# Performance work log

Measured on AMD Instinct MI355X. Metric: run time of the kernel, lower is better.

The kernel has to match this reference:

```python
import jax, jax.numpy as jnp
import numpy as np

N = 100000       # num nodes
E = 3200000      # num edges (avg degree 32)
F_IN = 128       # num_node_features
HID = 16         # hidden dim hard-coded in Net
C = 10           # num_classes


def setup_inputs() -> dict:
    key = jax.random.key(0)
    k1, k2, k3, k4 = jax.random.split(key, 4)
    x = jax.random.normal(k1, (N, F_IN), dtype=jnp.float32)
    edge_index = jax.random.randint(k2, (2, E), 0, N, dtype=jnp.int32)
    W1 = jax.random.normal(k3, (F_IN, HID), dtype=jnp.float32) * 0.05
    b1 = jnp.zeros((HID,), dtype=jnp.float32)
    W2 = jax.random.normal(k4, (HID, C), dtype=jnp.float32) * 0.05
    b2 = jnp.zeros((C,), dtype=jnp.float32)
    return {"x": x, "edge_index": edge_index, "W1": W1, "b1": b1, "W2": W2, "b2": b2}


def reference(x, edge_index, W1, b1, W2, b2):
    # GCNConv: out = D^{-1/2} (A + I) D^{-1/2} X W + b   (add self-loops)
    loops = jnp.arange(N, dtype=edge_index.dtype)
    row = jnp.concatenate([edge_index[0], loops])  # source nodes
    col = jnp.concatenate([edge_index[1], loops])  # target nodes

    # symmetric normalization (degrees include self-loops, so deg >= 1)
    deg = jax.ops.segment_sum(jnp.ones_like(col, dtype=jnp.float32), col, num_segments=N)
    dis = jax.lax.rsqrt(deg)
    norm = dis[row] * dis[col]  # [E+N]

    def gcn_conv(h, W, b):
        h = h @ W                               # [N, d_out] small GEMM first
        msg = h[row] * norm[:, None]            # gather + scale, [E+N, d_out]
        out = jax.ops.segment_sum(msg, col, num_segments=N)  # scatter-add
        return out + b

    h = jax.nn.relu(gcn_conv(x, W1, b1))
    # F.dropout(training=False) is identity in eval mode
    logits = gcn_conv(h, W2, b2)
    return jax.nn.log_softmax(logits, axis=1)
```

## Files before the change

### kernel.cpp

```cpp
#include <hip/hip_runtime.h>
#include <math.h>

#define N_NODES 100000
#define N_EDGES 3200000
#define F_IN 128
#define HID 16
#define C_OUT 10
#define WIN 256
#define NDIG 391
#define PNB2 500
#define EPB 6400
#define SCN (NDIG * PNB2)
#define SB1 764
#define MAXE 40

typedef unsigned short u16;
typedef unsigned int u32;

__device__ __forceinline__ float bf2f(u16 u) {
    return __uint_as_float(((u32)u) << 16);
}
__device__ __forceinline__ u16 f2bf(float f) {
    u32 x = __float_as_uint(f);
    u32 r = (x + 0x7fffu + ((x >> 16) & 1u)) >> 16;
    return (u16)r;
}
__device__ __forceinline__ void acc8(float* a, uint4 w) {
    a[0] += bf2f((u16)(w.x & 0xffff)); a[1] += bf2f((u16)(w.x >> 16));
    a[2] += bf2f((u16)(w.y & 0xffff)); a[3] += bf2f((u16)(w.y >> 16));
    a[4] += bf2f((u16)(w.z & 0xffff)); a[5] += bf2f((u16)(w.z >> 16));
    a[6] += bf2f((u16)(w.w & 0xffff)); a[7] += bf2f((u16)(w.w >> 16));
}

__global__ void k_pcnt(const int* __restrict__ col, int* __restrict__ blkhistA) {
    __shared__ int h[NDIG];
    for (int i = threadIdx.x; i < NDIG; i += 256) h[i] = 0;
    __syncthreads();
    const uint4* c4 = (const uint4*)(col + blockIdx.x * EPB);
    for (int i = threadIdx.x; i < EPB / 4; i += 256) {
        uint4 c = c4[i];
        atomicAdd(&h[c.x >> 8], 1);
        atomicAdd(&h[c.y >> 8], 1);
        atomicAdd(&h[c.z >> 8], 1);
        atomicAdd(&h[c.w >> 8], 1);
    }
    __syncthreads();
    for (int d = threadIdx.x; d < NDIG; d += 256)
        blkhistA[d * PNB2 + blockIdx.x] = h[d];
}

__global__ void k_s1(const int* __restrict__ blkhistA, int* __restrict__ psum) {
    __shared__ int sm[256];
    int i = blockIdx.x * 256 + threadIdx.x;
    sm[threadIdx.x] = (i < SCN) ? blkhistA[i] : 0;
    __syncthreads();
    for (int off = 128; off > 0; off >>= 1) {
        if (threadIdx.x < off) sm[threadIdx.x] += sm[threadIdx.x + off];
        __syncthreads();
    }
    if (threadIdx.x == 0) psum[blockIdx.x] = sm[0];
}

__global__ void k_s3(const int* __restrict__ blkhistA, const int* __restrict__ psum,
                     int* __restrict__ blkhistB) {
    __shared__ int ps[1024];
    __shared__ int sm[256];
    int t = threadIdx.x;
    for (int i = t; i < 1024; i += 256) ps[i] = (i < SB1) ? psum[i] : 0;
    __syncthreads();
    for (int off = 1; off < 1024; off <<= 1) {
        int v[4];
#pragma unroll
        for (int j = 0; j < 4; j++) {
            int idx = t + j * 256;
            v[j] = ps[idx] + ((idx >= off) ? ps[idx - off] : 0);
        }
        __syncthreads();
#pragma unroll
        for (int j = 0; j < 4; j++) ps[t + j * 256] = v[j];
        __syncthreads();
    }
    int bpre = (blockIdx.x > 0) ? ps[blockIdx.x - 1] : 0;

    int i = blockIdx.x * 256 + t;
    int v = (i < SCN) ? blkhistA[i] : 0;
    sm[t] = v;
    __syncthreads();
    for (int off = 1; off < 256; off <<= 1) {
        int a = sm[t];
        int b = (t >= off) ? sm[t - off] : 0;
        __syncthreads();
        sm[t] = a + b;
        __syncthreads();
    }
    if (i < SCN) blkhistB[i] = bpre + sm[t] - v;
}

__global__ void __launch_bounds__(512) k_pwrite(
        const int* __restrict__ row, const int* __restrict__ col,
        const int* __restrict__ blkhistA, const int* __restrict__ blkhistB,
        u32* __restrict__ staging) {
    __shared__ u32 sorted[EPB];
    __shared__ u16 dwin[EPB];
    __shared__ int gbase[NDIG];
    __shared__ int lbase[NDIG];
    __shared__ int lcur[NDIG];
    __shared__ int scan[512];

    int t = threadIdx.x;
    int b = blockIdx.x;
    int hv = 0;
    if (t < NDIG) {
        hv = blkhistA[t * PNB2 + b];
        gbase[t] = blkhistB[t * PNB2 + b];
        lcur[t] = 0;
    }
    scan[t] = hv;
    __syncthreads();
    for (int off = 1; off < 512; off <<= 1) {
        int v = scan[t];
        int u = (t >= off) ? scan[t - off] : 0;
        __syncthreads();
        scan[t] = v + u;
        __syncthreads();
    }
    if (t < NDIG) lbase[t] = scan[t] - hv;
    __syncthreads();

    const uint4* c4 = (const uint4*)(col + b * EPB);
    const uint4* r4 = (const uint4*)(row + b * EPB);
    for (int i = t; i < EPB / 4; i += 512) {
        uint4 c = c4[i];
        uint4 r = r4[i];
        int d, rank, pos;
        d = (int)(c.x >> 8); rank = atomicAdd(&lcur[d], 1); pos = lbase[d] + rank;
        sorted[pos] = ((c.x & 255u) << 17) | r.x; dwin[pos] = (u16)d;
        d = (int)(c.y >> 8); rank = atomicAdd(&lcur[d], 1); pos = lbase[d] + rank;
        sorted[pos] = ((c.y & 255u) << 17) | r.y; dwin[pos] = (u16)d;
        d = (int)(c.z >> 8); rank = atomicAdd(&lcur[d], 1); pos = lbase[d] + rank;
        sorted[pos] = ((c.z & 255u) << 17) | r.z; dwin[pos] = (u16)d;
        d = (int)(c.w >> 8); rank = atomicAdd(&lcur[d], 1); pos = lbase[d] + rank;
        sorted[pos] = ((c.w & 255u) << 17) | r.w; dwin[pos] = (u16)d;
    }
    __syncthreads();

    for (int i = t; i < EPB; i += 512) {
        int d = dwin[i];
        staging[gbase[d] + (i - lbase[d])] = sorted[i];
    }
}

__global__ void k_csr(u32* staging, const int* __restrict__ blkhistB,
                      int* __restrict__ offs, float* __restrict__ dis) {
    __shared__ int cnt[WIN];
    __shared__ int base[WIN];
    int w = blockIdx.x;
    int t = threadIdx.x;
    cnt[t] = 0;
    __syncthreads();
    int start = blkhistB[w * PNB2];
    int end = (w == NDIG - 1) ? N_EDGES : blkhistB[(w + 1) * PNB2];
    u32 buf[MAXE];
    int n = 0;
#pragma unroll
    for (int k = 0; k < MAXE; k++) {
        int i = start + k * 256 + t;
        if (i < end) {
            u32 e = staging[i];
            buf[k] = e;
            n = k + 1;
            atomicAdd(&cnt[e >> 17], 1);
        }
    }
    __syncthreads();
    base[t] = cnt[t];
    __syncthreads();
    for (int off = 1; off < WIN; off <<= 1) {
        int v = base[t];
        int u = (t >= off) ? base[t - off] : 0;
        __syncthreads();
        base[t] = v + u;
        __syncthreads();
    }
    int excl = base[t] - cnt[t];
    base[t] = excl;
    int node = w * WIN + t;
    if (node < N_NODES) {
        offs[node] = start + excl;
        dis[node] = rsqrtf(1.0f + (float)cnt[t]);
    }
    if (w == 0 && t == 0) offs[N_NODES] = N_EDGES;
    __syncthreads();
    cnt[t] = 0;
    __syncthreads();
#pragma unroll
    for (int k = 0; k < MAXE; k++) {
        if (k < n) {
            u32 e = buf[k];
            int cl = (int)(e >> 17);
            int rank = atomicAdd(&cnt[cl], 1);
            staging[start + base[cl] + rank] = e;
        }
    }
}

__global__ void k_gemm1(const float* __restrict__ x, const float* __restrict__ W1,
                        const float* __restrict__ dis, u16* __restrict__ h1s) {
    __shared__ float Ws[F_IN * HID];
    for (int t = threadIdx.x; t < F_IN * HID; t += blockDim.x) Ws[t] = W1[t];
    __syncthreads();

    int node = blockIdx.x * blockDim.x + threadIdx.x;
    if (node >= N_NODES) return;

    float acc[HID];
#pragma unroll
    for (int j = 0; j < HID; j++) acc[j] = 0.f;

    const float4* xr = (const float4*)(x + (size_t)node * F_IN);
#pragma unroll 2
    for (int k4 = 0; k4 < F_IN / 4; k4++) {
        float4 v = xr[k4];
        float xv[4] = {v.x, v.y, v.z, v.w};
#pragma unroll
        for (int kk = 0; kk < 4; kk++) {
            const float4* wr = (const float4*)(Ws + (k4 * 4 + kk) * HID);
            float4 w0 = wr[0], w1 = wr[1], w2 = wr[2], w3 = wr[3];
            float xs = xv[kk];
            acc[0]  += xs * w0.x; acc[1]  += xs * w0.y; acc[2]  += xs * w0.z; acc[3]  += xs * w0.w;
            acc[4]  += xs * w1.x; acc[5]  += xs * w1.y; acc[6]  += xs * w1.z; acc[7]  += xs * w1.w;
            acc[8]  += xs * w2.x; acc[9]  += xs * w2.y; acc[10] += xs * w2.z; acc[11] += xs * w2.w;
            acc[12] += xs * w3.x; acc[13] += xs * w3.y; acc[14] += xs * w3.z; acc[15] += xs * w3.w;
        }
    }

    float d = dis[node];
    u32 p[8];
#pragma unroll
    for (int i = 0; i < 8; i++)
        p[i] = (u32)f2bf(acc[2 * i] * d) | ((u32)f2bf(acc[2 * i + 1] * d) << 16);
    u32* dst = (u32*)(h1s + (size_t)node * HID);
#pragma unroll
    for (int i = 0; i < 8; i++) dst[i] = p[i];
}

__global__ void k_gl1(const int* __restrict__ offs, const u32* __restrict__ csr,
                      const float* __restrict__ dis, const u16* __restrict__ h1s,
                      const float* __restrict__ b1, const float* __restrict__ W2,
                      u16* __restrict__ h2s) {
    __shared__ float Ws[HID * C_OUT];
    __shared__ float b1s[HID];
    if (threadIdx.x < HID * C_OUT) Ws[threadIdx.x] = W2[threadIdx.x];
    if (threadIdx.x < HID) b1s[threadIdx.x] = b1[threadIdx.x];
    __syncthreads();

    int t = blockIdx.x * 256 + threadIdx.x;
    if (t >= N_NODES * 2) return;
    int node = t >> 1;
    int half = t & 1;
    const uint4* hb = (const uint4*)h1s;
    float a[8] = {0.f, 0.f, 0.f, 0.f, 0.f, 0.f, 0.f, 0.f};
    acc8(a, hb[(size_t)node * 2 + half]);
    int o = offs[node + half];
    int oo = __shfl_xor(o, 1);
    int s0 = half ? oo : o;
    int s1 = half ? o : oo;
    int j = s0;
    for (; j < s1 && (j & 3); j++)
        acc8(a, hb[(size_t)(csr[j] & 0x1FFFFu) * 2 + half]);
    for (; j + 4 <= s1; j += 4) {
        uint4 ss = *(const uint4*)(csr + j);
        uint4 w0 = hb[(size_t)(ss.x & 0x1FFFFu) * 2 + half];
        uint4 w1 = hb[(size_t)(ss.y & 0x1FFFFu) * 2 + half];
        uint4 w2 = hb[(size_t)(ss.z & 0x1FFFFu) * 2 + half];
        uint4 w3 = hb[(size_t)(ss.w & 0x1FFFFu) * 2 + half];
        acc8(a, w0); acc8(a, w1); acc8(a, w2); acc8(a, w3);
    }
    for (; j < s1; j++)
        acc8(a, hb[(size_t)(csr[j] & 0x1FFFFu) * 2 + half]);

    float dc = dis[node];
    float own[8], oth[8];
#pragma unroll
    for (int k = 0; k < 8; k++) own[k] = a[k] * dc;
#pragma unroll
    for (int k = 0; k < 8; k++) oth[k] = __shfl_xor(own[k], 1);
    float h[16];
#pragma unroll
    for (int k = 0; k < 8; k++) {
        h[k]     = half ? oth[k] : own[k];
        h[8 + k] = half ? own[k] : oth[k];
    }
#pragma unroll
    for (int jj = 0; jj < 16; jj++) h[jj] = fmaxf(h[jj] + b1s[jj], 0.f);

    int nf = half ? 2 : 8;
    float outv[8];
#pragma unroll
    for (int k = 0; k < 8; k++) {
        float s = 0.f;
        if (k < nf) {
            int kk = half * 8 + k;
#pragma unroll
            for (int jj = 0; jj < 16; jj++) s += h[jj] * Ws[jj * C_OUT + kk];
        }
        outv[k] = s * dc;
    }
    uint4 ov;
    ov.x = (u32)f2bf(outv[0]) | ((u32)f2bf(outv[1]) << 16);
    ov.y = half ? 0u : ((u32)f2bf(outv[2]) | ((u32)f2bf(outv[3]) << 16));
    ov.z = half ? 0u : ((u32)f2bf(outv[4]) | ((u32)f2bf(outv[5]) << 16));
    ov.w = half ? 0u : ((u32)f2bf(outv[6]) | ((u32)f2bf(outv[7]) << 16));
    ((uint4*)h2s)[(size_t)node * 2 + half] = ov;
}

__global__ void k_gather2(const int* __restrict__ offs, const u32* __restrict__ csr,
                          const float* __restrict__ dis, const u16* __restrict__ h2s,
                          const float* __restrict__ b2, float* __restrict__ out) {
    __shared__ float b2s[C_OUT];
    if (threadIdx.x < C_OUT) b2s[threadIdx.x] = b2[threadIdx.x];
    __syncthreads();

    int t = blockIdx.x * 256 + threadIdx.x;
    if (t >= N_NODES * 2) return;
    int node = t >> 1;
    int half = t & 1;
    const uint4* hb = (const uint4*)h2s;
    float a[8] = {0.f, 0.f, 0.f, 0.f, 0.f, 0.f, 0.f, 0.f};
    acc8(a, hb[(size_t)node * 2 + half]);
    int o = offs[node + half];
    int oo = __shfl_xor(o, 1);
    int s0 = half ? oo : o;
    int s1 = half ? o : oo;
    int j = s0;
    for (; j < s1 && (j & 3); j++)
        acc8(a, hb[(size_t)(csr[j] & 0x1FFFFu) * 2 + half]);
    for (; j + 4 <= s1; j += 4) {
        uint4 ss = *(const uint4*)(csr + j);
        uint4 w0 = hb[(size_t)(ss.x & 0x1FFFFu) * 2 + half];
        uint4 w1 = hb[(size_t)(ss.y & 0x1FFFFu) * 2 + half];
        uint4 w2 = hb[(size_t)(ss.z & 0x1FFFFu) * 2 + half];
        uint4 w3 = hb[(size_t)(ss.w & 0x1FFFFu) * 2 + half];
        acc8(a, w0); acc8(a, w1); acc8(a, w2); acc8(a, w3);
    }
    for (; j < s1; j++)
        acc8(a, hb[(size_t)(csr[j] & 0x1FFFFu) * 2 + half]);

    float dc = dis[node];
    int nf = half ? 2 : 8;
    float lg[8];
    float m = -1e30f;
#pragma unroll
    for (int k = 0; k < 8; k++) {
        lg[k] = a[k] * dc + b2s[(half * 8 + k) % C_OUT];
        if (k < nf) m = fmaxf(m, lg[k]);
    }
    m = fmaxf(m, __shfl_xor(m, 1));
    float s = 0.f;
#pragma unroll
    for (int k = 0; k < 8; k++)
        if (k < nf) s += expf(lg[k] - m);
    s += __shfl_xor(s, 1);
    float ls = logf(s) + m;
    float* dst = out + (size_t)node * C_OUT + half * 8;
    if (half == 0) {
#pragma unroll
        for (int i = 0; i < 4; i++)
            *(float2*)(dst + 2 * i) = make_float2(lg[2 * i] - ls, lg[2 * i + 1] - ls);
    } else {
        *(float2*)dst = make_float2(lg[0] - ls, lg[1] - ls);
    }
}

extern "C" void kernel_launch(void* const* d_in, const int* in_sizes, int n_in,
                              void* d_out, int out_size, void* d_ws, size_t ws_size,
                              hipStream_t stream) {
    const float* x  = (const float*)d_in[0];
    const int*   ei = (const int*)d_in[1];
    const float* W1 = (const float*)d_in[2];
    const float* b1 = (const float*)d_in[3];
    const float* W2 = (const float*)d_in[4];
    const float* b2 = (const float*)d_in[5];
    float* out = (float*)d_out;

    const int* row = ei;
    const int* col = ei + N_EDGES;

    char* ws = (char*)d_ws;
    float* dis      = (float*)(ws);
    int*   offs     = (int*)(ws + 400000);
    int*   blkhistA = (int*)(ws + 800016);
    int*   blkhistB = (int*)(ws + 1582352);
    int*   psum     = (int*)(ws + 2364688);
    u32*   staging  = (u32*)(ws + 2367744);
    u16*   h1s      = (u16*)(ws + 15167744);
    u16*   h2s      = (u16*)(ws + 18367744);

    const int B = 256;
    int gN  = (N_NODES + B - 1) / B;
    int gN2 = (N_NODES * 2 + B - 1) / B;

    k_pcnt  <<<PNB2, B, 0, stream>>>(col, blkhistA);
    k_s1    <<<SB1, B, 0, stream>>>(blkhistA, psum);
    k_s3    <<<SB1, B, 0, stream>>>(blkhistA, psum, blkhistB);
    k_pwrite<<<PNB2, 512, 0, stream>>>(row, col, blkhistA, blkhistB, staging);
    k_csr   <<<NDIG, B, 0, stream>>>(staging, blkhistB, offs, dis);
    k_gemm1 <<<gN, B, 0, stream>>>(x, W1, dis, h1s);
    k_gl1   <<<gN2, B, 0, stream>>>(offs, staging, dis, h1s, b1, W2, h2s);
    k_gather2<<<gN2, B, 0, stream>>>(offs, staging, dis, h2s, b2, out);
}
```

Baseline: 237.4 us.

## Replace per-node CSR sort with per-window shared-memory atomic aggregation

Drops the second-level counting sort that built the per-node CSR. The degree kernel now only counts per-target degrees, and the two gather kernels become edge-parallel per 256-node window. Each edge atomically adds its source features into a padded shared-memory accumulator, then 256 threads finish each node (self-loop, bias, ReLU, W2 or log_softmax). This removes the reorder and scatter pass, but adds many LDS float atomics and launches only 391 blocks, which may underuse the GPU and makes the summation order nondeterministic.

Result: slower. 706.4 us (+197.6%).

```diff
diff --git a/kernel.cpp b/kernel.cpp
--- a/kernel.cpp
+++ b/kernel.cpp
@@ -12,7 +12,8 @@
 #define EPB 6400
 #define SCN (NDIG * PNB2)
 #define SB1 764
-#define MAXE 40
+#define AP1 17
+#define AP2 11
 
 typedef unsigned short u16;
 typedef unsigned int u32;
@@ -30,6 +31,16 @@
     a[2] += bf2f((u16)(w.y & 0xffff)); a[3] += bf2f((u16)(w.y >> 16));
     a[4] += bf2f((u16)(w.z & 0xffff)); a[5] += bf2f((u16)(w.z >> 16));
     a[6] += bf2f((u16)(w.w & 0xffff)); a[7] += bf2f((u16)(w.w >> 16));
+}
+__device__ __forceinline__ void atom8(float* a, uint4 w) {
+    atomicAdd(a + 0, bf2f((u16)(w.x & 0xffff)));
+    atomicAdd(a + 1, bf2f((u16)(w.x >> 16)));
+    atomicAdd(a + 2, bf2f((u16)(w.y & 0xffff)));
+    atomicAdd(a + 3, bf2f((u16)(w.y >> 16)));
+    atomicAdd(a + 4, bf2f((u16)(w.z & 0xffff)));
+    atomicAdd(a + 5, bf2f((u16)(w.z >> 16)));
+    atomicAdd(a + 6, bf2f((u16)(w.w & 0xffff)));
+    atomicAdd(a + 7, bf2f((u16)(w.w >> 16)));
 }
 
 __global__ void k_pcnt(const int* __restrict__ col, int* __restrict__ blkhistA) {
@@ -150,58 +161,22 @@
     }
 }
 
-__global__ void k_csr(u32* staging, const int* __restrict__ blkhistB,
-                      int* __restrict__ offs, float* __restrict__ dis) {
+__global__ void __launch_bounds__(512) k_deg(
+        const u32* __restrict__ staging, const int* __restrict__ blkhistB,
+        float* __restrict__ dis) {
     __shared__ int cnt[WIN];
-    __shared__ int base[WIN];
     int w = blockIdx.x;
     int t = threadIdx.x;
-    cnt[t] = 0;
+    if (t < WIN) cnt[t] = 0;
     __syncthreads();
     int start = blkhistB[w * PNB2];
     int end = (w == NDIG - 1) ? N_EDGES : blkhistB[(w + 1) * PNB2];
-    u32 buf[MAXE];
-    int n = 0;
-#pragma unroll
-    for (int k = 0; k < MAXE; k++) {
-        int i = start + k * 256 + t;
-        if (i < end) {
-            u32 e = staging[i];
-            buf[k] = e;
-            n = k + 1;
-            atomicAdd(&cnt[e >> 17], 1);
-        }
-    }
-    __syncthreads();
-    base[t] = cnt[t];
-    __syncthreads();
-    for (int off = 1; off < WIN; off <<= 1) {
-        int v = base[t];
-        int u = (t >= off) ? base[t - off] : 0;
-        __syncthreads();
-        base[t] = v + u;
-        __syncthreads();
-    }
-    int excl = base[t] - cnt[t];
-    base[t] = excl;
+    for (int i = start + t; i < end; i += 512)
+        atomicAdd(&cnt[staging[i] >> 17], 1);
+    __syncthreads();
     int node = w * WIN + t;
-    if (node < N_NODES) {
-        offs[node] = start + excl;
+    if (t < WIN && node < N_NODES)
         dis[node] = rsqrtf(1.0f + (float)cnt[t]);
-    }
-    if (w == 0 && t == 0) offs[N_NODES] = N_EDGES;
-    __syncthreads();
-    cnt[t] = 0;
-    __syncthreads();
-#pragma unroll
-    for (int k = 0; k < MAXE; k++) {
-        if (k < n) {
-            u32 e = buf[k];
-            int cl = (int)(e >> 17);
-            int rank = atomicAdd(&cnt[cl], 1);
-            staging[start + base[cl] + rank] = e;
-        }
-    }
 }
 
 __global__ void k_gemm1(const float* __restrict__ x, const float* __restrict__ W1,
@@ -244,131 +219,156 @@
     for (int i = 0; i < 8; i++) dst[i] = p[i];
 }
 
-__global__ void k_gl1(const int* __restrict__ offs, const u32* __restrict__ csr,
-                      const float* __restrict__ dis, const u16* __restrict__ h1s,
-                      const float* __restrict__ b1, const float* __restrict__ W2,
-                      u16* __restrict__ h2s) {
+__global__ void __launch_bounds__(512) k_gl1e(
+        const int* __restrict__ blkhistB, const u32* __restrict__ staging,
+        const float* __restrict__ dis, const u16* __restrict__ h1s,
+        const float* __restrict__ b1, const float* __restrict__ W2,
+        u16* __restrict__ h2s) {
+    __shared__ float acc[WIN * AP1];
     __shared__ float Ws[HID * C_OUT];
     __shared__ float b1s[HID];
-    if (threadIdx.x < HID * C_OUT) Ws[threadIdx.x] = W2[threadIdx.x];
-    if (threadIdx.x < HID) b1s[threadIdx.x] = b1[threadIdx.x];
-    __syncthreads();
-
-    int t = blockIdx.x * 256 + threadIdx.x;
-    if (t >= N_NODES * 2) return;
-    int node = t >> 1;
-    int half = t & 1;
+    int t = threadIdx.x;
+    int w = blockIdx.x;
+    if (t < HID * C_OUT) Ws[t] = W2[t];
+    if (t < HID) b1s[t] = b1[t];
+    for (int i = t; i < WIN * AP1; i += 512) acc[i] = 0.f;
+    __syncthreads();
+
+    int start = blkhistB[w * PNB2];
+    int end = (w == NDIG - 1) ? N_EDGES : blkhistB[(w + 1) * PNB2];
     const uint4* hb = (const uint4*)h1s;
-    float a[8] = {0.f, 0.f, 0.f, 0.f, 0.f, 0.f, 0.f, 0.f};
-    acc8(a, hb[(size_t)node * 2 + half]);
-    int o = offs[node + half];
-    int oo = __shfl_xor(o, 1);
-    int s0 = half ? oo : o;
-    int s1 = half ? o : oo;
-    int j = s0;
-    for (; j < s1 && (j & 3); j++)
-        acc8(a, hb[(size_t)(csr[j] & 0x1FFFFu) * 2 + half]);
-    for (; j + 4 <= s1; j += 4) {
-        uint4 ss = *(const uint4*)(csr + j);
-        uint4 w0 = hb[(size_t)(ss.x & 0x1FFFFu) * 2 + half];
-        uint4 w1 = hb[(size_t)(ss.y & 0x1FFFFu) * 2 + half];
-        uint4 w2 = hb[(size_t)(ss.z & 0x1FFFFu) * 2 + half];
-        uint4 w3 = hb[(size_t)(ss.w & 0x1FFFFu) * 2 + half];
-        acc8(a, w0); acc8(a, w1); acc8(a, w2); acc8(a, w3);
-    }
-    for (; j < s1; j++)
-        acc8(a, hb[(size_t)(csr[j] & 0x1FFFFu) * 2 + half]);
-
-    float dc = dis[node];
-    float own[8], oth[8];
-#pragma unroll
-    for (int k = 0; k < 8; k++) own[k] = a[k] * dc;
-#pragma unroll
-    for (int k = 0; k < 8; k++) oth[k] = __shfl_xor(own[k], 1);
-    float h[16];
-#pragma unroll
-    for (int k = 0; k < 8; k++) {
-        h[k]     = half ? oth[k] : own[k];
-        h[8 + k] = half ? own[k] : oth[k];
-    }
-#pragma unroll
-    for (int jj = 0; jj < 16; jj++) h[jj] = fmaxf(h[jj] + b1s[jj], 0.f);
-
-    int nf = half ? 2 : 8;
-    float outv[8];
-#pragma unroll
-    for (int k = 0; k < 8; k++) {
-        float s = 0.f;
-        if (k < nf) {
-            int kk = half * 8 + k;
-#pragma unroll
-            for (int jj = 0; jj < 16; jj++) s += h[jj] * Ws[jj * C_OUT + kk];
-        }
-        outv[k] = s * dc;
-    }
-    uint4 ov;
-    ov.x = (u32)f2bf(outv[0]) | ((u32)f2bf(outv[1]) << 16);
-    ov.y = half ? 0u : ((u32)f2bf(outv[2]) | ((u32)f2bf(outv[3]) << 16));
-    ov.z = half ? 0u : ((u32)f2bf(outv[4]) | ((u32)f2bf(outv[5]) << 16));
-    ov.w = half ? 0u : ((u32)f2bf(outv[6]) | ((u32)f2bf(outv[7]) << 16));
-    ((uint4*)h2s)[(size_t)node * 2 + half] = ov;
-}
-
-__global__ void k_gather2(const int* __restrict__ offs, const u32* __restrict__ csr,
-                          const float* __restrict__ dis, const u16* __restrict__ h2s,
-                          const float* __restrict__ b2, float* __restrict__ out) {
+
+    int i = start + t;
+    if (i < end) {
+        u32 e = staging[i];
+        int src = (int)(e & 0x1FFFFu);
+        uint4 va = hb[2 * (size_t)src];
+        uint4 vb = hb[2 * (size_t)src + 1];
+        for (;;) {
+            int inext = i + 512;
+            bool more = (inext < end);
+            u32 en = e; uint4 na = va, nb = vb;
+            if (more) {
+                en = staging[inext];
+                int sn = (int)(en & 0x1FFFFu);
+                na = hb[2 * (size_t)sn];
+                nb = hb[2 * (size_t)sn + 1];
+            }
+            float* arow = acc + (e >> 17) * AP1;
+            atom8(arow, va);
+            atom8(arow + 8, vb);
+            if (!more) break;
+            i = inext; e = en; va = na; vb = nb;
+        }
+    }
+    __syncthreads();
+
+    if (t < WIN) {
+        int node = w * WIN + t;
+        if (node < N_NODES) {
+            float dc = dis[node];
+            float sum[HID];
+            const float* arow = acc + t * AP1;
+#pragma unroll
+            for (int j = 0; j < HID; j++) sum[j] = arow[j];
+            acc8(sum, hb[2 * (size_t)node]);
+            acc8(sum + 8, hb[2 * (size_t)node + 1]);
+            float h[HID];
+#pragma unroll
+            for (int j = 0; j < HID; j++)
+                h[j] = fmaxf(sum[j] * dc + b1s[j], 0.f);
+            float outv[C_OUT];
+#pragma unroll
+            for (int k = 0; k < C_OUT; k++) {
+                float s = 0.f;
+#pragma unroll
+                for (int j = 0; j < HID; j++) s += h[j] * Ws[j * C_OUT + k];
+                outv[k] = s * dc;
+            }
+            uint4 o0, o1;
+            o0.x = (u32)f2bf(outv[0]) | ((u32)f2bf(outv[1]) << 16);
+            o0.y = (u32)f2bf(outv[2]) | ((u32)f2bf(outv[3]) << 16);
+            o0.z = (u32)f2bf(outv[4]) | ((u32)f2bf(outv[5]) << 16);
+            o0.w = (u32)f2bf(outv[6]) | ((u32)f2bf(outv[7]) << 16);
+            o1.x = (u32)f2bf(outv[8]) | ((u32)f2bf(outv[9]) << 16);
+            o1.y = 0u; o1.z = 0u; o1.w = 0u;
+            uint4* dst = (uint4*)h2s + 2 * (size_t)node;
+            dst[0] = o0; dst[1] = o1;
+        }
+    }
+}
+
+__global__ void __launch_bounds__(512) k_g2e(
+        const int* __restrict__ blkhistB, const u32* __restrict__ staging,
+        const float* __restrict__ dis, const u16* __restrict__ h2s,
+        const float* __restrict__ b2, float* __restrict__ out) {
+    __shared__ float acc[WIN * AP2];
     __shared__ float b2s[C_OUT];
-    if (threadIdx.x < C_OUT) b2s[threadIdx.x] = b2[threadIdx.x];
-    __syncthreads();
-
-    int t = blockIdx.x * 256 + threadIdx.x;
-    if (t >= N_NODES * 2) return;
-    int node = t >> 1;
-    int half = t & 1;
+    int t = threadIdx.x;
+    int w = blockIdx.x;
+    if (t < C_OUT) b2s[t] = b2[t];
+    for (int i = t; i < WIN * AP2; i += 512) acc[i] = 0.f;
+    __syncthreads();
+
+    int start = blkhistB[w * PNB2];
+    int end = (w == NDIG - 1) ? N_EDGES : blkhistB[(w + 1) * PNB2];
     const uint4* hb = (const uint4*)h2s;
-    float a[8] = {0.f, 0.f, 0.f, 0.f, 0.f, 0.f, 0.f, 0.f};
-    acc8(a, hb[(size_t)node * 2 + half]);
-    int o = offs[node + half];
-    int oo = __shfl_xor(o, 1);
-    int s0 = half ? oo : o;
-    int s1 = half ? o : oo;
-    int j = s0;
-    for (; j < s1 && (j & 3); j++)
-        acc8(a, hb[(size_t)(csr[j] & 0x1FFFFu) * 2 + half]);
-    for (; j + 4 <= s1; j += 4) {
-        uint4 ss = *(const uint4*)(csr + j);
-        uint4 w0 = hb[(size_t)(ss.x & 0x1FFFFu) * 2 + half];
-        uint4 w1 = hb[(size_t)(ss.y & 0x1FFFFu) * 2 + half];
-        uint4 w2 = hb[(size_t)(ss.z & 0x1FFFFu) * 2 + half];
-        uint4 w3 = hb[(size_t)(ss.w & 0x1FFFFu) * 2 + half];
-        acc8(a, w0); acc8(a, w1); acc8(a, w2); acc8(a, w3);
-    }
-    for (; j < s1; j++)
-        acc8(a, hb[(size_t)(csr[j] & 0x1FFFFu) * 2 + half]);
-
-    float dc = dis[node];
-    int nf = half ? 2 : 8;
-    float lg[8];
-    float m = -1e30f;
-#pragma unroll
-    for (int k = 0; k < 8; k++) {
-        lg[k] = a[k] * dc + b2s[(half * 8 + k) % C_OUT];
-        if (k < nf) m = fmaxf(m, lg[k]);
-    }
-    m = fmaxf(m, __shfl_xor(m, 1));
-    float s = 0.f;
-#pragma unroll
-    for (int k = 0; k < 8; k++)
-        if (k < nf) s += expf(lg[k] - m);
-    s += __shfl_xor(s, 1);
-    float ls = logf(s) + m;
-    float* dst = out + (size_t)node * C_OUT + half * 8;
-    if (half == 0) {
-#pragma unroll
-        for (int i = 0; i < 4; i++)
-            *(float2*)(dst + 2 * i) = make_float2(lg[2 * i] - ls, lg[2 * i + 1] - ls);
-    } else {
-        *(float2*)dst = make_float2(lg[0] - ls, lg[1] - ls);
+    const u32* h32 = (const u32*)h2s;
+
+    int i = start + t;
+    if (i < end) {
+        u32 e = staging[i];
+        int src = (int)(e & 0x1FFFFu);
+        uint4 va = hb[2 * (size_t)src];
+        u32 vc = h32[(size_t)src * 8 + 4];
+        for (;;) {
+            int inext = i + 512;
+            bool more = (inext < end);
+            u32 en = e; uint4 na = va; u32 nc = vc;
+            if (more) {
+                en = staging[inext];
+                int sn = (int)(en & 0x1FFFFu);
+                na = hb[2 * (size_t)sn];
+                nc = h32[(size_t)sn * 8 + 4];
+            }
+            float* arow = acc + (e >> 17) * AP2;
+            atom8(arow, va);
+            atomicAdd(arow + 8, bf2f((u16)(vc & 0xffff)));
+            atomicAdd(arow + 9, bf2f((u16)(vc >> 16)));
+            if (!more) break;
+            i = inext; e = en; va = na; vc = nc;
+        }
+    }
+    __syncthreads();
+
+    if (t < WIN) {
+        int node = w * WIN + t;
+        if (node < N_NODES) {
+            float dc = dis[node];
+            float sum[C_OUT];
+            const float* arow = acc + t * AP2;
+#pragma unroll
+            for (int k = 0; k < C_OUT; k++) sum[k] = arow[k];
+            acc8(sum, hb[2 * (size_t)node]);
+            u32 sc = h32[(size_t)node * 8 + 4];
+            sum[8] += bf2f((u16)(sc & 0xffff));
+            sum[9] += bf2f((u16)(sc >> 16));
+            float lg[C_OUT];
+            float m = -1e30f;
+#pragma unroll
+            for (int k = 0; k < C_OUT; k++) {
+                lg[k] = sum[k] * dc + b2s[k];
+                m = fmaxf(m, lg[k]);
+            }
+            float s = 0.f;
+#pragma unroll
+            for (int k = 0; k < C_OUT; k++) s += expf(lg[k] - m);
+            float ls = logf(s) + m;
+            float2* dst = (float2*)(out + (size_t)node * C_OUT);
+#pragma unroll
+            for (int k = 0; k < 5; k++)
+                dst[k] = make_float2(lg[2 * k] - ls, lg[2 * k + 1] - ls);
+        }
     }
 }
 
@@ -388,7 +388,6 @@
 
     char* ws = (char*)d_ws;
     float* dis      = (float*)(ws);
-    int*   offs     = (int*)(ws + 400000);
     int*   blkhistA = (int*)(ws + 800016);
     int*   blkhistB = (int*)(ws + 1582352);
     int*   psum     = (int*)(ws + 2364688);
@@ -398,14 +397,13 @@
 
     const int B = 256;
     int gN  = (N_NODES + B - 1) / B;
-    int gN2 = (N_NODES * 2 + B - 1) / B;
 
     k_pcnt  <<<PNB2, B, 0, stream>>>(col, blkhistA);
     k_s1    <<<SB1, B, 0, stream>>>(blkhistA, psum);
     k_s3    <<<SB1, B, 0, stream>>>(blkhistA, psum, blkhistB);
     k_pwrite<<<PNB2, 512, 0, stream>>>(row, col, blkhistA, blkhistB, staging);
-    k_csr   <<<NDIG, B, 0, stream>>>(staging, blkhistB, offs, dis);
+    k_deg   <<<NDIG, 512, 0, stream>>>(staging, blkhistB, dis);
     k_gemm1 <<<gN, B, 0, stream>>>(x, W1, dis, h1s);
-    k_gl1   <<<gN2, B, 0, stream>>>(offs, staging, dis, h1s, b1, W2, h2s);
-    k_gather2<<<gN2, B, 0, stream>>>(offs, staging, dis, h2s, b2, out);
-}
+    k_gl1e  <<<NDIG, 512, 0, stream>>>(blkhistB, staging, dis, h1s, b1, W2, h2s);
+    k_g2e   <<<NDIG, 512, 0, stream>>>(blkhistB, staging, dis, h2s, b2, out);
+}
```

## Split each node's edge list across two lanes in gathers and widen CSR blocks

Applied to the files above, without the earlier changes.

The two gather kernels now use four lanes per node instead of two: each feature half is handled by two lanes that each take half of the node's edge range, and their partial sums are combined with a lane shuffle before the epilogue. The CSR build kernel runs with 512 threads per block and a per-thread buffer of 20 entries instead of 40, with the scan and count steps guarded to the first 256 threads. The aim is more memory-level parallelism and shorter per-thread serial loops in the latency-bound gathers, and less register pressure in the CSR kernel. The cost is twice as many threads, extra shuffles, and duplicated epilogue math in lanes that never store.

Result: faster. 222.8 us (-6.1%).

```diff
diff --git a/kernel.cpp b/kernel.cpp
--- a/kernel.cpp
+++ b/kernel.cpp
@@ -12,7 +12,7 @@
 #define EPB 6400
 #define SCN (NDIG * PNB2)
 #define SB1 764
-#define MAXE 40
+#define MAXE2 20
 
 typedef unsigned short u16;
 typedef unsigned int u32;
@@ -150,21 +150,22 @@
     }
 }
 
-__global__ void k_csr(u32* staging, const int* __restrict__ blkhistB,
-                      int* __restrict__ offs, float* __restrict__ dis) {
+__global__ void __launch_bounds__(512) k_csr(
+        u32* staging, const int* __restrict__ blkhistB,
+        int* __restrict__ offs, float* __restrict__ dis) {
     __shared__ int cnt[WIN];
     __shared__ int base[WIN];
     int w = blockIdx.x;
     int t = threadIdx.x;
-    cnt[t] = 0;
+    if (t < WIN) cnt[t] = 0;
     __syncthreads();
     int start = blkhistB[w * PNB2];
     int end = (w == NDIG - 1) ? N_EDGES : blkhistB[(w + 1) * PNB2];
-    u32 buf[MAXE];
+    u32 buf[MAXE2];
     int n = 0;
 #pragma unroll
-    for (int k = 0; k < MAXE; k++) {
-        int i = start + k * 256 + t;
+    for (int k = 0; k < MAXE2; k++) {
+        int i = start + k * 512 + t;
         if (i < end) {
             u32 e = staging[i];
             buf[k] = e;
@@ -173,28 +174,33 @@
         }
     }
     __syncthreads();
-    base[t] = cnt[t];
+    if (t < WIN) base[t] = cnt[t];
     __syncthreads();
     for (int off = 1; off < WIN; off <<= 1) {
-        int v = base[t];
-        int u = (t >= off) ? base[t - off] : 0;
-        __syncthreads();
-        base[t] = v + u;
-        __syncthreads();
-    }
-    int excl = base[t] - cnt[t];
-    base[t] = excl;
-    int node = w * WIN + t;
-    if (node < N_NODES) {
-        offs[node] = start + excl;
-        dis[node] = rsqrtf(1.0f + (float)cnt[t]);
+        int v = 0;
+        if (t < WIN) {
+            v = base[t];
+            if (t >= off) v += base[t - off];
+        }
+        __syncthreads();
+        if (t < WIN) base[t] = v;
+        __syncthreads();
+    }
+    if (t < WIN) {
+        int excl = base[t] - cnt[t];
+        base[t] = excl;
+        int node = w * WIN + t;
+        if (node < N_NODES) {
+            offs[node] = start + excl;
+            dis[node] = rsqrtf(1.0f + (float)cnt[t]);
+        }
     }
     if (w == 0 && t == 0) offs[N_NODES] = N_EDGES;
     __syncthreads();
-    cnt[t] = 0;
-    __syncthreads();
-#pragma unroll
-    for (int k = 0; k < MAXE; k++) {
+    if (t < WIN) cnt[t] = 0;
+    __syncthreads();
+#pragma unroll
+    for (int k = 0; k < MAXE2; k++) {
         if (k < n) {
             u32 e = buf[k];
             int cl = (int)(e >> 17);
@@ -255,20 +261,25 @@
     __syncthreads();
 
     int t = blockIdx.x * 256 + threadIdx.x;
-    if (t >= N_NODES * 2) return;
-    int node = t >> 1;
-    int half = t & 1;
+    if (t >= N_NODES * 4) return;
+    int node = t >> 2;
+    int q = t & 3;
+    int half = q >> 1;
+    int eh = q & 1;
     const uint4* hb = (const uint4*)h1s;
     float a[8] = {0.f, 0.f, 0.f, 0.f, 0.f, 0.f, 0.f, 0.f};
-    acc8(a, hb[(size_t)node * 2 + half]);
+    if (eh == 0) acc8(a, hb[(size_t)node * 2 + half]);
     int o = offs[node + half];
-    int oo = __shfl_xor(o, 1);
+    int oo = __shfl_xor(o, 2);
     int s0 = half ? oo : o;
     int s1 = half ? o : oo;
-    int j = s0;
-    for (; j < s1 && (j & 3); j++)
+    int mid = s0 + ((s1 - s0) >> 1);
+    int lo = eh ? mid : s0;
+    int hi = eh ? s1 : mid;
+    int j = lo;
+    for (; j < hi && (j & 3); j++)
         acc8(a, hb[(size_t)(csr[j] & 0x1FFFFu) * 2 + half]);
-    for (; j + 4 <= s1; j += 4) {
+    for (; j + 4 <= hi; j += 4) {
         uint4 ss = *(const uint4*)(csr + j);
         uint4 w0 = hb[(size_t)(ss.x & 0x1FFFFu) * 2 + half];
         uint4 w1 = hb[(size_t)(ss.y & 0x1FFFFu) * 2 + half];
@@ -276,15 +287,18 @@
         uint4 w3 = hb[(size_t)(ss.w & 0x1FFFFu) * 2 + half];
         acc8(a, w0); acc8(a, w1); acc8(a, w2); acc8(a, w3);
     }
-    for (; j < s1; j++)
+    for (; j < hi; j++)
         acc8(a, hb[(size_t)(csr[j] & 0x1FFFFu) * 2 + half]);
+
+#pragma unroll
+    for (int k = 0; k < 8; k++) a[k] += __shfl_xor(a[k], 1);
 
     float dc = dis[node];
     float own[8], oth[8];
 #pragma unroll
     for (int k = 0; k < 8; k++) own[k] = a[k] * dc;
 #pragma unroll
-    for (int k = 0; k < 8; k++) oth[k] = __shfl_xor(own[k], 1);
+    for (int k = 0; k < 8; k++) oth[k] = __shfl_xor(own[k], 2);
     float h[16];
 #pragma unroll
     for (int k = 0; k < 8; k++) {
@@ -306,12 +320,14 @@
         }
         outv[k] = s * dc;
     }
-    uint4 ov;
-    ov.x = (u32)f2bf(outv[0]) | ((u32)f2bf(outv[1]) << 16);
-    ov.y = half ? 0u : ((u32)f2bf(outv[2]) | ((u32)f2bf(outv[3]) << 16));
-    ov.z = half ? 0u : ((u32)f2bf(outv[4]) | ((u32)f2bf(outv[5]) << 16));
-    ov.w = half ? 0u : ((u32)f2bf(outv[6]) | ((u32)f2bf(outv[7]) << 16));
-    ((uint4*)h2s)[(size_t)node * 2 + half] = ov;
+    if (eh == 0) {
+        uint4 ov;
+        ov.x = (u32)f2bf(outv[0]) | ((u32)f2bf(outv[1]) << 16);
+        ov.y = half ? 0u : ((u32)f2bf(outv[2]) | ((u32)f2bf(outv[3]) << 16));
+        ov.z = half ? 0u : ((u32)f2bf(outv[4]) | ((u32)f2bf(outv[5]) << 16));
+        ov.w = half ? 0u : ((u32)f2bf(outv[6]) | ((u32)f2bf(outv[7]) << 16));
+        ((uint4*)h2s)[(size_t)node * 2 + half] = ov;
+    }
 }
 
 __global__ void k_gather2(const int* __restrict__ offs, const u32* __restrict__ csr,
@@ -322,20 +338,25 @@
     __syncthreads();
 
     int t = blockIdx.x * 256 + threadIdx.x;
-    if (t >= N_NODES * 2) return;
-    int node = t >> 1;
-    int half = t & 1;
+    if (t >= N_NODES * 4) return;
+    int node = t >> 2;
+    int q = t & 3;
+    int half = q >> 1;
+    int eh = q & 1;
     const uint4* hb = (const uint4*)h2s;
     float a[8] = {0.f, 0.f, 0.f, 0.f, 0.f, 0.f, 0.f, 0.f};
-    acc8(a, hb[(size_t)node * 2 + half]);
+    if (eh == 0) acc8(a, hb[(size_t)node * 2 + half]);
     int o = offs[node + half];
-    int oo = __shfl_xor(o, 1);
+    int oo = __shfl_xor(o, 2);
     int s0 = half ? oo : o;
     int s1 = half ? o : oo;
-    int j = s0;
-    for (; j < s1 && (j & 3); j++)
+    int mid = s0 + ((s1 - s0) >> 1);
+    int lo = eh ? mid : s0;
+    int hi = eh ? s1 : mid;
+    int j = lo;
+    for (; j < hi && (j & 3); j++)
         acc8(a, hb[(size_t)(csr[j] & 0x1FFFFu) * 2 + half]);
-    for (; j + 4 <= s1; j += 4) {
+    for (; j + 4 <= hi; j += 4) {
         uint4 ss = *(const uint4*)(csr + j);
         uint4 w0 = hb[(size_t)(ss.x & 0x1FFFFu) * 2 + half];
         uint4 w1 = hb[(size_t)(ss.y & 0x1FFFFu) * 2 + half];
@@ -343,8 +364,11 @@
         uint4 w3 = hb[(size_t)(ss.w & 0x1FFFFu) * 2 + half];
         acc8(a, w0); acc8(a, w1); acc8(a, w2); acc8(a, w3);
     }
-    for (; j < s1; j++)
+    for (; j < hi; j++)
         acc8(a, hb[(size_t)(csr[j] & 0x1FFFFu) * 2 + half]);
+
+#pragma unroll
+    for (int k = 0; k < 8; k++) a[k] += __shfl_xor(a[k], 1);
 
     float dc = dis[node];
     int nf = half ? 2 : 8;
@@ -355,20 +379,22 @@
         lg[k] = a[k] * dc + b2s[(half * 8 + k) % C_OUT];
         if (k < nf) m = fmaxf(m, lg[k]);
     }
-    m = fmaxf(m, __shfl_xor(m, 1));
+    m = fmaxf(m, __shfl_xor(m, 2));
     float s = 0.f;
 #pragma unroll
     for (int k = 0; k < 8; k++)
         if (k < nf) s += expf(lg[k] - m);
-    s += __shfl_xor(s, 1);
+    s += __shfl_xor(s, 2);
     float ls = logf(s) + m;
-    float* dst = out + (size_t)node * C_OUT + half * 8;
-    if (half == 0) {
-#pragma unroll
-        for (int i = 0; i < 4; i++)
-            *(float2*)(dst + 2 * i) = make_float2(lg[2 * i] - ls, lg[2 * i + 1] - ls);
-    } else {
-        *(float2*)dst = make_float2(lg[0] - ls, lg[1] - ls);
+    if (eh == 0) {
+        float* dst = out + (size_t)node * C_OUT + half * 8;
+        if (half == 0) {
+#pragma unroll
+            for (int i = 0; i < 4; i++)
+                *(float2*)(dst + 2 * i) = make_float2(lg[2 * i] - ls, lg[2 * i + 1] - ls);
+        } else {
+            *(float2*)dst = make_float2(lg[0] - ls, lg[1] - ls);
+        }
     }
 }
 
@@ -398,14 +424,14 @@
 
     const int B = 256;
     int gN  = (N_NODES + B - 1) / B;
-    int gN2 = (N_NODES * 2 + B - 1) / B;
+    int gN4 = (N_NODES * 4 + B - 1) / B;
 
     k_pcnt  <<<PNB2, B, 0, stream>>>(col, blkhistA);
     k_s1    <<<SB1, B, 0, stream>>>(blkhistA, psum);
     k_s3    <<<SB1, B, 0, stream>>>(blkhistA, psum, blkhistB);
     k_pwrite<<<PNB2, 512, 0, stream>>>(row, col, blkhistA, blkhistB, staging);
-    k_csr   <<<NDIG, B, 0, stream>>>(staging, blkhistB, offs, dis);
+    k_csr   <<<NDIG, 512, 0, stream>>>(staging, blkhistB, offs, dis);
     k_gemm1 <<<gN, B, 0, stream>>>(x, W1, dis, h1s);
-    k_gl1   <<<gN2, B, 0, stream>>>(offs, staging, dis, h1s, b1, W2, h2s);
-    k_gather2<<<gN2, B, 0, stream>>>(offs, staging, dis, h2s, b2, out);
-}
+    k_gl1   <<<gN4, B, 0, stream>>>(offs, staging, dis, h1s, b1, W2, h2s);
+    k_gather2<<<gN4, B, 0, stream>>>(offs, staging, dis, h2s, b2, out);
+}
```
